# Kernel optimization log

Hardware: AMD Instinct MI355X
Metric: run time of the kernel (lower is better)

## Reference

```python
import jax, jax.numpy as jnp
import numpy as np

LMAX = 10
F_IN = 64
F_OUT = 64
N_GRID = 512
IRREP_DIM = sum((2 * l + 1) ** 2 for l in range(LMAX + 1))  # 1771
BATCH = 256


def setup_inputs() -> dict:
    key = jax.random.key(0)
    kx, kD, kw = jax.random.split(key, 3)
    x = jax.random.normal(kx, (BATCH, F_IN, IRREP_DIM), dtype=jnp.float32)
    D = jax.random.normal(kD, (N_GRID, IRREP_DIM), dtype=jnp.float32)
    w = jax.random.normal(kw, (F_IN, F_OUT, N_GRID), dtype=jnp.float32)
    return {"x": x, "D": D, "w": w}


def _so3_linear(x, psi):
    # x:   (B, f_in, sum_l (2l+1)^2) signal over SO(3) irreps
    # psi: (f_in, f_out, sum_l (2l+1)^2) per-degree block weights
    B, f_in, _ = x.shape
    f_out = psi.shape[1]
    outs = []
    off = 0
    for l in range(LMAX + 1):
        d = 2 * l + 1
        blk = d * d
        # input block: multiplicity u (=d) x irrep component m (=d)
        x_l = x[:, :, off:off + blk].reshape(B, f_in, d, d)        # (B,i,u,m)
        w_l = psi[:, :, off:off + blk].reshape(f_in, f_out, d, d)  # (i,o,u,v)
        alpha = 1.0 / np.sqrt(f_in * d)  # e3nn fan-in path normalization
        out_l = jnp.einsum('bium,iouv->bovm', x_l, w_l) * alpha
        outs.append(out_l.reshape(B, f_out, blk))
        off += blk
    return jnp.concatenate(outs, axis=-1)


def reference(x, D, w):
    # project spatial filter into Fourier (irrep) domain
    n_grid = D.shape[0]
    psi = jnp.einsum('ni,xyn->xyi', D, w) / np.sqrt(n_grid)  # (f_in, f_out, IRREP_DIM)
    return _so3_linear(x, psi)
```

## Files before the change

### kernel.cpp

```cpp
#include <hip/hip_runtime.h>
#include <hip/hip_bf16.h>

#define IDIM 1771
#define NF 64
#define NG 512

constexpr int OFFS[12] = {0, 1, 10, 35, 84, 165, 286, 455, 680, 969, 1330, 1771};

typedef float f32x4 __attribute__((ext_vector_type(4)));
typedef float f32x2 __attribute__((ext_vector_type(2)));
typedef __bf16 bf16x2 __attribute__((ext_vector_type(2)));
typedef __bf16 bf16x8 __attribute__((ext_vector_type(8)));

__device__ __forceinline__ void gl_lds16(const void* g, void* l) {
    __builtin_amdgcn_global_load_lds((const __attribute__((address_space(1))) void*)g,
                                     (__attribute__((address_space(3))) void*)l, 16, 0, 0);
}

__global__ __launch_bounds__(256) void prep_dw_kernel(const float* __restrict__ D,
                                                      const float* __restrict__ w,
                                                      __bf16* __restrict__ Dt,
                                                      __bf16* __restrict__ wb) {
    __shared__ alignas(16) float T[64][65];
    const int blk = blockIdx.x;
    const int t = threadIdx.x;
    const int lane = t & 63, grp = t >> 6;

    if (blk < 224) {
        const int ct = blk >> 3, nt = blk & 7;
        const int c0 = ct * 64, n0 = nt * 64;
        float tmp[16];
#pragma unroll
        for (int p = 0; p < 16; ++p) {
            int nn = grp + p * 4;
            int c = c0 + lane;
            tmp[p] = (c < IDIM) ? D[(size_t)(n0 + nn) * IDIM + c] : 0.0f;
        }
#pragma unroll
        for (int p = 0; p < 16; ++p) T[grp + p * 4][lane] = tmp[p];
        __syncthreads();
        for (int cc = grp; cc < 64; cc += 4) {
            int c = c0 + cc;
            if (c < IDIM) Dt[c * NG + n0 + lane] = (__bf16)T[lane][cc];
        }
    } else {
        const int o = blk - 224;
#pragma unroll
        for (int ii0 = 0; ii0 < 64; ii0 += 8) {
            f32x2 tmp[8];
#pragma unroll
            for (int j = 0; j < 8; ++j)
                tmp[j] = *(const f32x2*)&w[((size_t)((ii0 + j) * 64 + o)) * NG + t * 2];
#pragma unroll
            for (int j = 0; j < 8; ++j) {
                bf16x2 ov;
                ov.x = (__bf16)tmp[j].x;
                ov.y = (__bf16)tmp[j].y;
                *(bf16x2*)&wb[((size_t)(o * 64 + ii0 + j)) * NG + t * 2] = ov;
            }
        }
    }
}

__global__ __launch_bounds__(256) void repack_x_kernel(const float* __restrict__ x,
                                                       __hip_bfloat16* __restrict__ A) {
    __shared__ alignas(16) __bf16 T[64][66];
    const int idx = blockIdx.x;
    const int l = idx >> 8;
    const int b = idx & 255;
    const int t = threadIdx.x;
    const int lane = t & 63, grp = t >> 6;
    const int d = 2 * l + 1, off = OFFS[l], csq = d * d, Kp = 64 * d;
    const float* xb = x + (size_t)b * NF * IDIM + off;
    __bf16* Ab = (__bf16*)(A + (size_t)16384 * off + (size_t)b * d * Kp);

    for (int c0 = 0; c0 < csq; c0 += 64) {
        float tmp[16];
#pragma unroll
        for (int p = 0; p < 16; ++p) {
            int ii = grp + p * 4;
            int c = c0 + lane;
            tmp[p] = (c < csq) ? xb[(size_t)ii * IDIM + c] : 0.0f;
        }
#pragma unroll
        for (int p = 0; p < 16; ++p) T[grp + p * 4][lane] = (__bf16)tmp[p];
        __syncthreads();
#pragma unroll
        for (int s = 0; s < 2; ++s) {
            int idx2 = s * 256 + t;
            int c_loc = idx2 >> 3, i0 = (idx2 & 7) * 8;
            int c = c0 + c_loc;
            if (c < csq) {
                int u = (unsigned)c / (unsigned)d;
                int m = c - u * d;
                bf16x8 v;
#pragma unroll
                for (int j = 0; j < 8; ++j) v[j] = T[i0 + j][c_loc];
                *(bf16x8*)(Ab + (size_t)m * Kp + u * 64 + i0) = v;
            }
        }
        __syncthreads();
    }
}

__global__ __launch_bounds__(256) void psi_mfma_kernel(const __bf16* __restrict__ Dt,
                                                       const __bf16* __restrict__ wb,
                                                       __bf16* __restrict__ Bm) {
    __shared__ alignas(16) __bf16 S[2 * 16384];

    const int t = threadIdx.x, w = t >> 6, ln = t & 63;
    const int row0 = blockIdx.x * 128;
    const int col0 = blockIdx.y * 128;

    const bool isA = (w < 2);
    const int wsub = w & 1;
    const int rowloc = ln >> 3;
    const int logslot = (ln & 7) ^ rowloc;

    const __bf16* gp[8];
    __bf16* lp[8];
#pragma unroll
    for (int q = 0; q < 8; ++q) {
        int chunk = wsub * 8 + q;
        int row = chunk * 8 + rowloc;
        int g = isA ? (row0 + row < IDIM ? row0 + row : IDIM - 1) : (col0 + row);
        gp[q] = (isA ? Dt : wb) + (size_t)g * NG + logslot * 8;
        lp[q] = S + (isA ? 0 : 8192) + chunk * 512;
    }

    f32x4 acc[4][4];
    f32x4 zero = {0.0f, 0.0f, 0.0f, 0.0f};
#pragma unroll
    for (int i = 0; i < 4; ++i)
#pragma unroll
        for (int j = 0; j < 4; ++j) acc[i][j] = zero;

    const int wr = (w >> 1) * 64, wc = (w & 1) * 64;
    const int fr = ln & 15, kh = ln >> 4;
    const int fx = fr & 7;

    int aoff[2][4], boff[2][4];
#pragma unroll
    for (int kk = 0; kk < 2; ++kk)
#pragma unroll
        for (int mt = 0; mt < 4; ++mt) {
            aoff[kk][mt] = (wr + mt * 16 + fr) * 64 + (((kk << 2) | kh) ^ fx) * 8;
            boff[kk][mt] = (wc + mt * 16 + fr) * 64 + (((kk << 2) | kh) ^ fx) * 8;
        }

    const int np = NG / 64;

#pragma unroll
    for (int q = 0; q < 8; ++q) { gl_lds16(gp[q], lp[q]); gp[q] += 64; }
    asm volatile("s_waitcnt vmcnt(0)" ::: "memory");
    __builtin_amdgcn_s_barrier();
    __builtin_amdgcn_sched_barrier(0);

    int bi = 0;
    for (int p = 0; p < np; ++p) {
        if (p + 1 < np) {
#pragma unroll
            for (int q = 0; q < 8; ++q) {
                gl_lds16(gp[q], lp[q] + (bi ^ 1) * 16384);
                gp[q] += 64;
            }
        }
        const __bf16* As_ = S + bi * 16384;
        const __bf16* Bs_ = As_ + 8192;
        bf16x8 af[2][4], bf_[2][4];
#pragma unroll
        for (int kk = 0; kk < 2; ++kk) {
#pragma unroll
            for (int mt = 0; mt < 4; ++mt) af[kk][mt] = *(const bf16x8*)&As_[aoff[kk][mt]];
#pragma unroll
            for (int nt = 0; nt < 4; ++nt) bf_[kk][nt] = *(const bf16x8*)&Bs_[boff[kk][nt]];
        }
#pragma unroll
        for (int kk = 0; kk < 2; ++kk)
#pragma unroll
            for (int mt = 0; mt < 4; ++mt)
#pragma unroll
                for (int nt = 0; nt < 4; ++nt)
                    acc[mt][nt] = __builtin_amdgcn_mfma_f32_16x16x32_bf16(
                        af[kk][mt], bf_[kk][nt], acc[mt][nt], 0, 0, 0);
        asm volatile("s_waitcnt vmcnt(0)" ::: "memory");
        __builtin_amdgcn_s_barrier();
        __builtin_amdgcn_sched_barrier(0);
        bi ^= 1;
    }

    const float sc = 0.04419417382415922f;
    const int o = (col0 + wc) >> 6;
#pragma unroll
    for (int mt = 0; mt < 4; ++mt) {
#pragma unroll
        for (int e = 0; e < 4; ++e) {
            int c = row0 + wr + mt * 16 + kh * 4 + e;
            if (c < IDIM) {
                int l = 0;
#pragma unroll
                for (int ll = 1; ll < 11; ++ll)
                    if (c >= OFFS[ll]) l = ll;
                int d = 2 * l + 1, off = OFFS[l];
                int rem = c - off;
                int u = (unsigned)rem / (unsigned)d;
                int v = rem - u * d;
                __bf16* bb = Bm + (size_t)4096 * off + (size_t)(o * d + v) * (64 * d) + u * 64;
#pragma unroll
                for (int nt = 0; nt < 4; ++nt) {
                    int i = nt * 16 + fr;
                    bb[i] = (__bf16)(acc[mt][nt][e] * sc);
                }
            }
        }
    }
}

__global__ __launch_bounds__(256) void so3_gemm_all(const __bf16* __restrict__ A,
                                                    const __bf16* __restrict__ Bm,
                                                    float* __restrict__ out) {
    const int bid = blockIdx.x;
    const int v_ = (bid & 7) * 237 + (bid >> 3);
    if (v_ >= 1892) return;

    int l = 10, base = 0;
    if (v_ >= 462)  { l = 9; base = 462; }
    if (v_ >= 842)  { l = 8; base = 842; }
    if (v_ >= 1148) { l = 7; base = 1148; }
    if (v_ >= 1388) { l = 6; base = 1388; }
    if (v_ >= 1570) { l = 5; base = 1570; }
    if (v_ >= 1702) { l = 4; base = 1702; }
    if (v_ >= 1792) { l = 3; base = 1792; }
    if (v_ >= 1848) { l = 2; base = 1848; }
    if (v_ >= 1878) { l = 1; base = 1878; }
    if (v_ >= 1890) { l = 0; base = 1890; }

    const int d = 2 * l + 1;
    const int off = OFFS[l];
    const int Np = 64 * d, Kp = 64 * d;
    const int ntiles = l + 1;
    const int rel = v_ - base;
    const int bx = (unsigned)rel / (unsigned)ntiles;
    const int by = rel - bx * ntiles;
    const int row0 = bx * 128, col0 = by * 128;

    constexpr float ALPHA[11] = {0.125f, 0.07216878f, 0.05590170f, 0.04724556f,
                                 0.04166667f, 0.03768892f, 0.03466879f, 0.03227486f,
                                 0.03031695f, 0.02867697f, 0.02727724f};

    __shared__ alignas(16) __bf16 S[2 * 16384];

    const int t = threadIdx.x, w = t >> 6, ln = t & 63;

    const __bf16* Abase = A + (size_t)16384 * off;
    const __bf16* Bbase = Bm + (size_t)4096 * off;

    const bool isA = (w < 2);
    const int wsub = w & 1;
    const int rowloc = ln >> 3;
    const int logslot = (ln & 7) ^ rowloc;

    const __bf16* gp[8];
    __bf16* lp[8];
#pragma unroll
    for (int q = 0; q < 8; ++q) {
        int chunk = wsub * 8 + q;
        int row = chunk * 8 + rowloc;
        int g = isA ? (row0 + row) : (col0 + row < Np ? col0 + row : Np - 1);
        gp[q] = (isA ? Abase : Bbase) + (size_t)g * Kp + logslot * 8;
        lp[q] = S + (isA ? 0 : 8192) + chunk * 512;
    }

    f32x4 acc[4][4];
    f32x4 zero = {0.0f, 0.0f, 0.0f, 0.0f};
#pragma unroll
    for (int i = 0; i < 4; ++i)
#pragma unroll
        for (int j = 0; j < 4; ++j) acc[i][j] = zero;

    const int wr = (w >> 1) * 64, wc = (w & 1) * 64;
    const int fr = ln & 15, kh = ln >> 4;
    const int fx = fr & 7;

    int aoff[2][4], boff[2][4];
#pragma unroll
    for (int kk = 0; kk < 2; ++kk)
#pragma unroll
        for (int mt = 0; mt < 4; ++mt) {
            aoff[kk][mt] = (wr + mt * 16 + fr) * 64 + (((kk << 2) | kh) ^ fx) * 8;
            boff[kk][mt] = (wc + mt * 16 + fr) * 64 + (((kk << 2) | kh) ^ fx) * 8;
        }

    const int np = Kp / 64;

#pragma unroll
    for (int q = 0; q < 8; ++q) { gl_lds16(gp[q], lp[q]); gp[q] += 64; }
    asm volatile("s_waitcnt vmcnt(0)" ::: "memory");
    __builtin_amdgcn_s_barrier();
    __builtin_amdgcn_sched_barrier(0);

    int bi = 0;
    for (int p = 0; p < np; ++p) {
        if (p + 1 < np) {
#pragma unroll
            for (int q = 0; q < 8; ++q) {
                gl_lds16(gp[q], lp[q] + (bi ^ 1) * 16384);
                gp[q] += 64;
            }
        }
        const __bf16* As_ = S + bi * 16384;
        const __bf16* Bs_ = As_ + 8192;
        bf16x8 af[2][4], bf_[2][4];
#pragma unroll
        for (int kk = 0; kk < 2; ++kk) {
#pragma unroll
            for (int mt = 0; mt < 4; ++mt) af[kk][mt] = *(const bf16x8*)&As_[aoff[kk][mt]];
#pragma unroll
            for (int nt = 0; nt < 4; ++nt) bf_[kk][nt] = *(const bf16x8*)&Bs_[boff[kk][nt]];
        }
#pragma unroll
        for (int kk = 0; kk < 2; ++kk)
#pragma unroll
            for (int mt = 0; mt < 4; ++mt)
#pragma unroll
                for (int nt = 0; nt < 4; ++nt)
                    acc[mt][nt] = __builtin_amdgcn_mfma_f32_16x16x32_bf16(
                        af[kk][mt], bf_[kk][nt], acc[mt][nt], 0, 0, 0);
        asm volatile("s_waitcnt vmcnt(0)" ::: "memory");
        __builtin_amdgcn_s_barrier();
        __builtin_amdgcn_sched_barrier(0);
        bi ^= 1;
    }

    __syncthreads();
    float* Tw = (float*)S + w * 256;
    const float alpha = ALPHA[l];

#pragma unroll
    for (int mt = 0; mt < 4; ++mt) {
        int r = row0 + wr + mt * 16 + fr;
        int b = (unsigned)r / (unsigned)d;
        int m = r - b * d;
        float* ob = out + (size_t)b * NF * IDIM + off + m;
#pragma unroll
        for (int nt = 0; nt < 4; ++nt) {
#pragma unroll
            for (int e = 0; e < 4; ++e) Tw[(kh * 4 + e) * 16 + fr] = acc[mt][nt][e];
            f32x4 vals = *(const f32x4*)&Tw[fr * 16 + kh * 4];
            int qb = col0 + wc + nt * 16 + kh * 4;
            int o = (unsigned)qb / (unsigned)d;
            int vv = qb - o * d;
#pragma unroll
            for (int j = 0; j < 4; ++j) {
                if (qb + j < Np) ob[o * IDIM + vv * d] = alpha * vals[j];
                ++vv;
                if (vv == d) { vv = 0; ++o; }
            }
        }
    }
}

extern "C" void kernel_launch(void* const* d_in, const int* in_sizes, int n_in,
                              void* d_out, int out_size, void* d_ws, size_t ws_size,
                              hipStream_t stream) {
    const float* x = (const float*)d_in[0];
    const float* D = (const float*)d_in[1];
    const float* w = (const float*)d_in[2];
    float* out = (float*)d_out;

    char* ws = (char*)d_ws;
    const size_t DT_BYTES = (size_t)IDIM * NG * 2;
    const size_t WB_BYTES = (size_t)4096 * NG * 2;
    const size_t A_BYTES = (size_t)16384 * IDIM * 2;

    __bf16* Dt = (__bf16*)ws;
    __bf16* wb = (__bf16*)(ws + DT_BYTES);
    __hip_bfloat16* A = (__hip_bfloat16*)(ws + DT_BYTES + WB_BYTES);
    __bf16* Bm = (__bf16*)(ws + DT_BYTES + WB_BYTES + A_BYTES);

    prep_dw_kernel<<<288, 256, 0, stream>>>(D, w, Dt, wb);
    repack_x_kernel<<<2816, 256, 0, stream>>>(x, A);
    psi_mfma_kernel<<<dim3(14, 32), 256, 0, stream>>>(Dt, wb, Bm);
    so3_gemm_all<<<1896, 256, 0, stream>>>((const __bf16*)A, Bm, out);
}
```

Baseline: 379.5 us.

## Pre-swizzle A and B into MFMA fragment layout and load directly to registers

The repack and psi kernels now write A and B in a tiled layout: 16-row tiles by 64-wide K chunks, arranged so that each lane's bf16x8 MFMA fragment is contiguous. The main GEMM drops the LDS staging, the global_load_lds double buffer and the barriers. Each wave instead loads its fragments straight from global memory into registers, with a two-stage register prefetch. This removes LDS traffic and synchronisation, but each wave now fetches its A and B tiles separately with no sharing through LDS, so global/L2 traffic rises and register pressure grows.

```diff
diff --git a/kernel.cpp b/kernel.cpp
--- a/kernel.cpp
+++ b/kernel.cpp
@@ -63,16 +63,16 @@
 }
 
 __global__ __launch_bounds__(256) void repack_x_kernel(const float* __restrict__ x,
-                                                       __hip_bfloat16* __restrict__ A) {
+                                                       __bf16* __restrict__ A) {
     __shared__ alignas(16) __bf16 T[64][66];
     const int idx = blockIdx.x;
     const int l = idx >> 8;
     const int b = idx & 255;
     const int t = threadIdx.x;
     const int lane = t & 63, grp = t >> 6;
-    const int d = 2 * l + 1, off = OFFS[l], csq = d * d, Kp = 64 * d;
+    const int d = 2 * l + 1, off = OFFS[l], csq = d * d;
     const float* xb = x + (size_t)b * NF * IDIM + off;
-    __bf16* Ab = (__bf16*)(A + (size_t)16384 * off + (size_t)b * d * Kp);
+    __bf16* Al = A + (size_t)16384 * off;
 
     for (int c0 = 0; c0 < csq; c0 += 64) {
         float tmp[16];
@@ -93,10 +93,12 @@
             if (c < csq) {
                 int u = (unsigned)c / (unsigned)d;
                 int m = c - u * d;
+                int r = b * d + m;
                 bf16x8 v;
 #pragma unroll
                 for (int j = 0; j < 8; ++j) v[j] = T[i0 + j][c_loc];
-                *(bf16x8*)(Ab + (size_t)m * Kp + u * 64 + i0) = v;
+                *(bf16x8*)(Al + (size_t)((r >> 4) * d + u) * 1024 +
+                           (i0 >> 3) * 128 + (r & 15) * 8) = v;
             }
         }
         __syncthreads();
@@ -205,11 +207,13 @@
                 int rem = c - off;
                 int u = (unsigned)rem / (unsigned)d;
                 int v = rem - u * d;
-                __bf16* bb = Bm + (size_t)4096 * off + (size_t)(o * d + v) * (64 * d) + u * 64;
+                int col = o * d + v;
+                __bf16* bb = Bm + (size_t)4096 * off +
+                             (size_t)((col >> 4) * d + u) * 1024 + (col & 15) * 8;
 #pragma unroll
                 for (int nt = 0; nt < 4; ++nt) {
                     int i = nt * 16 + fr;
-                    bb[i] = (__bf16)(acc[mt][nt][e] * sc);
+                    bb[(i >> 3) * 128 + (i & 7)] = (__bf16)(acc[mt][nt][e] * sc);
                 }
             }
         }
@@ -237,7 +241,7 @@
 
     const int d = 2 * l + 1;
     const int off = OFFS[l];
-    const int Np = 64 * d, Kp = 64 * d;
+    const int Np = 64 * d;
     const int ntiles = l + 1;
     const int rel = v_ - base;
     const int bx = (unsigned)rel / (unsigned)ntiles;
@@ -248,27 +252,25 @@
                                  0.04166667f, 0.03768892f, 0.03466879f, 0.03227486f,
                                  0.03031695f, 0.02867697f, 0.02727724f};
 
-    __shared__ alignas(16) __bf16 S[2 * 16384];
+    __shared__ alignas(16) float TwS[4][256];
 
     const int t = threadIdx.x, w = t >> 6, ln = t & 63;
-
-    const __bf16* Abase = A + (size_t)16384 * off;
-    const __bf16* Bbase = Bm + (size_t)4096 * off;
-
-    const bool isA = (w < 2);
-    const int wsub = w & 1;
-    const int rowloc = ln >> 3;
-    const int logslot = (ln & 7) ^ rowloc;
-
-    const __bf16* gp[8];
-    __bf16* lp[8];
-#pragma unroll
-    for (int q = 0; q < 8; ++q) {
-        int chunk = wsub * 8 + q;
-        int row = chunk * 8 + rowloc;
-        int g = isA ? (row0 + row) : (col0 + row < Np ? col0 + row : Np - 1);
-        gp[q] = (isA ? Abase : Bbase) + (size_t)g * Kp + logslot * 8;
-        lp[q] = S + (isA ? 0 : 8192) + chunk * 512;
+    const int wr = (w >> 1) * 64, wc = (w & 1) * 64;
+    const int fr = ln & 15, kh = ln >> 4;
+
+    const int rT0 = (row0 + wr) >> 4;
+    const int cT0 = (col0 + wc) >> 4;
+    const __bf16* pA[4];
+    const __bf16* pB[4];
+#pragma unroll
+    for (int mt = 0; mt < 4; ++mt)
+        pA[mt] = A + (size_t)16384 * off + (size_t)(rT0 + mt) * d * 1024 + kh * 128 + fr * 8;
+#pragma unroll
+    for (int nt = 0; nt < 4; ++nt) {
+        int cT = cT0 + nt;
+        int cmax = 4 * d - 1;
+        if (cT > cmax) cT = cmax;
+        pB[nt] = Bm + (size_t)4096 * off + (size_t)cT * d * 1024 + kh * 128 + fr * 8;
     }
 
     f32x4 acc[4][4];
@@ -278,45 +280,26 @@
 #pragma unroll
         for (int j = 0; j < 4; ++j) acc[i][j] = zero;
 
-    const int wr = (w >> 1) * 64, wc = (w & 1) * 64;
-    const int fr = ln & 15, kh = ln >> 4;
-    const int fx = fr & 7;
-
-    int aoff[2][4], boff[2][4];
+    bf16x8 a0[2][4], b0[2][4], a1[2][4], b1[2][4];
 #pragma unroll
     for (int kk = 0; kk < 2; ++kk)
 #pragma unroll
-        for (int mt = 0; mt < 4; ++mt) {
-            aoff[kk][mt] = (wr + mt * 16 + fr) * 64 + (((kk << 2) | kh) ^ fx) * 8;
-            boff[kk][mt] = (wc + mt * 16 + fr) * 64 + (((kk << 2) | kh) ^ fx) * 8;
-        }
-
-    const int np = Kp / 64;
-
-#pragma unroll
-    for (int q = 0; q < 8; ++q) { gl_lds16(gp[q], lp[q]); gp[q] += 64; }
-    asm volatile("s_waitcnt vmcnt(0)" ::: "memory");
-    __builtin_amdgcn_s_barrier();
-    __builtin_amdgcn_sched_barrier(0);
-
-    int bi = 0;
-    for (int p = 0; p < np; ++p) {
-        if (p + 1 < np) {
-#pragma unroll
-            for (int q = 0; q < 8; ++q) {
-                gl_lds16(gp[q], lp[q] + (bi ^ 1) * 16384);
-                gp[q] += 64;
-            }
-        }
-        const __bf16* As_ = S + bi * 16384;
-        const __bf16* Bs_ = As_ + 8192;
-        bf16x8 af[2][4], bf_[2][4];
-#pragma unroll
-        for (int kk = 0; kk < 2; ++kk) {
-#pragma unroll
-            for (int mt = 0; mt < 4; ++mt) af[kk][mt] = *(const bf16x8*)&As_[aoff[kk][mt]];
-#pragma unroll
-            for (int nt = 0; nt < 4; ++nt) bf_[kk][nt] = *(const bf16x8*)&Bs_[boff[kk][nt]];
+        for (int q = 0; q < 4; ++q) {
+            a0[kk][q] = *(const bf16x8*)(pA[q] + kk * 512);
+            b0[kk][q] = *(const bf16x8*)(pB[q] + kk * 512);
+        }
+
+    const int np = d;
+    for (int p = 0; p < np; p += 2) {
+        const bool has1 = (p + 1 < np), has2 = (p + 2 < np);
+        if (has1) {
+#pragma unroll
+            for (int kk = 0; kk < 2; ++kk)
+#pragma unroll
+                for (int q = 0; q < 4; ++q) {
+                    a1[kk][q] = *(const bf16x8*)(pA[q] + 1024 + kk * 512);
+                    b1[kk][q] = *(const bf16x8*)(pB[q] + 1024 + kk * 512);
+                }
         }
 #pragma unroll
         for (int kk = 0; kk < 2; ++kk)
@@ -325,15 +308,31 @@
 #pragma unroll
                 for (int nt = 0; nt < 4; ++nt)
                     acc[mt][nt] = __builtin_amdgcn_mfma_f32_16x16x32_bf16(
-                        af[kk][mt], bf_[kk][nt], acc[mt][nt], 0, 0, 0);
-        asm volatile("s_waitcnt vmcnt(0)" ::: "memory");
-        __builtin_amdgcn_s_barrier();
-        __builtin_amdgcn_sched_barrier(0);
-        bi ^= 1;
-    }
-
-    __syncthreads();
-    float* Tw = (float*)S + w * 256;
+                        a0[kk][mt], b0[kk][nt], acc[mt][nt], 0, 0, 0);
+#pragma unroll
+        for (int q = 0; q < 4; ++q) { pA[q] += 2048; pB[q] += 2048; }
+        if (has2) {
+#pragma unroll
+            for (int kk = 0; kk < 2; ++kk)
+#pragma unroll
+                for (int q = 0; q < 4; ++q) {
+                    a0[kk][q] = *(const bf16x8*)(pA[q] + kk * 512);
+                    b0[kk][q] = *(const bf16x8*)(pB[q] + kk * 512);
+                }
+        }
+        if (has1) {
+#pragma unroll
+            for (int kk = 0; kk < 2; ++kk)
+#pragma unroll
+                for (int mt = 0; mt < 4; ++mt)
+#pragma unroll
+                    for (int nt = 0; nt < 4; ++nt)
+                        acc[mt][nt] = __builtin_amdgcn_mfma_f32_16x16x32_bf16(
+                            a1[kk][mt], b1[kk][nt], acc[mt][nt], 0, 0, 0);
+        }
+    }
+
+    float* Tw = &TwS[w][0];
     const float alpha = ALPHA[l];
 
 #pragma unroll
@@ -375,7 +374,7 @@
 
     __bf16* Dt = (__bf16*)ws;
     __bf16* wb = (__bf16*)(ws + DT_BYTES);
-    __hip_bfloat16* A = (__hip_bfloat16*)(ws + DT_BYTES + WB_BYTES);
+    __bf16* A = (__bf16*)(ws + DT_BYTES + WB_BYTES);
     __bf16* Bm = (__bf16*)(ws + DT_BYTES + WB_BYTES + A_BYTES);
 
     prep_dw_kernel<<<288, 256, 0, stream>>>(D, w, Dt, wb);
```

Measured after the change: 412.7 us. 1.09x slower.
